# Kernel tuning notes

Hardware: AMD Instinct MI355X
Metric: run time of the kernel (lower is better)

## Reference

```python
import jax, jax.numpy as jnp
import numpy as np

N_TX, N_CARD, N_MERCH = 200000, 50000, 10000
E = 200000
TX_IN, EMB, H = 128, 64, 128
N_LAYERS, N_ETYPES = 2, 4  # etypes: 0 card->tx, 1 tx->card, 2 merch->tx, 3 tx->merch


def setup_inputs() -> dict:
    key = jax.random.key(0)
    ks = jax.random.split(key, 24)
    s = 0.05
    inp = {
        "tx_x": jax.random.normal(ks[0], (N_TX, TX_IN), jnp.float32),
        "card_ids": jnp.arange(N_CARD, dtype=jnp.int64),
        "merch_ids": jnp.arange(N_MERCH, dtype=jnp.int64),
        "e_card": jax.random.randint(ks[1], (E,), 0, N_CARD),
        "e_tx_c": jnp.arange(E, dtype=jnp.int64),
        "e_merch": jax.random.randint(ks[2], (E,), 0, N_MERCH),
        "e_tx_m": jnp.arange(E, dtype=jnp.int64),
        # parameters
        "card_emb": jax.random.normal(ks[3], (N_CARD, EMB), jnp.float32) * s,
        "merch_emb": jax.random.normal(ks[4], (N_MERCH, EMB), jnp.float32) * s,
        "card_proj_W": jax.random.normal(ks[5], (EMB, H), jnp.float32) * s,
        "card_proj_b": jnp.zeros((H,), jnp.float32),
        "merch_proj_W": jax.random.normal(ks[6], (EMB, H), jnp.float32) * s,
        "merch_proj_b": jnp.zeros((H,), jnp.float32),
        "tx_W": jax.random.normal(ks[7], (TX_IN, H), jnp.float32) * s,
        "tx_b": jnp.zeros((H,), jnp.float32),
        "conv_Wl": jax.random.normal(ks[8], (N_LAYERS, N_ETYPES, H, H), jnp.float32) * s,
        "conv_bl": jnp.zeros((N_LAYERS, N_ETYPES, H), jnp.float32),
        "conv_Wr": jax.random.normal(ks[9], (N_LAYERS, N_ETYPES, H, H), jnp.float32) * s,
        "h1_W": jax.random.normal(ks[10], (H, H), jnp.float32) * s,
        "h1_b": jnp.zeros((H,), jnp.float32),
        "h2_W": jax.random.normal(ks[11], (H, 1), jnp.float32) * s,
        "h2_b": jnp.zeros((1,), jnp.float32),
    }
    return inp


def _sage(x_src, x_dst, src, dst, Wl, bl, Wr, n_dst):
    # PyG SAGEConv: mean-aggregate neighbor features, then lin_l(agg)+lin_r(x_dst)
    agg = jax.ops.segment_sum(x_src[src], dst, num_segments=n_dst)
    cnt = jax.ops.segment_sum(jnp.ones((src.shape[0],), x_src.dtype), dst, num_segments=n_dst)
    mean = agg / jnp.maximum(cnt, 1.0)[:, None]
    return mean @ Wl + bl + x_dst @ Wr


def reference(tx_x, card_ids, merch_ids, e_card, e_tx_c, e_merch, e_tx_m,
              card_emb, merch_emb, card_proj_W, card_proj_b, merch_proj_W, merch_proj_b,
              tx_W, tx_b, conv_Wl, conv_bl, conv_Wr, h1_W, h1_b, h2_W, h2_b):
    # input encoders (dropout inactive at eval)
    h_tx = jax.nn.relu(tx_x @ tx_W + tx_b)
    h_card = card_emb[card_ids] @ card_proj_W + card_proj_b
    h_merch = merch_emb[merch_ids] @ merch_proj_W + merch_proj_b

    for l in range(N_LAYERS):
        Wl, bl, Wr = conv_Wl[l], conv_bl[l], conv_Wr[l]
        # HeteroConv aggr='sum' across edge types sharing a dst type
        o_tx = (_sage(h_card, h_tx, e_card, e_tx_c, Wl[0], bl[0], Wr[0], N_TX)
                + _sage(h_merch, h_tx, e_merch, e_tx_m, Wl[2], bl[2], Wr[2], N_TX))
        o_card = _sage(h_tx, h_card, e_tx_c, e_card, Wl[1], bl[1], Wr[1], N_CARD)
        o_merch = _sage(h_tx, h_merch, e_tx_m, e_merch, Wl[3], bl[3], Wr[3], N_MERCH)
        h_tx, h_card, h_merch = jax.nn.relu(o_tx), jax.nn.relu(o_card), jax.nn.relu(o_merch)

    logits = (jax.nn.relu(h_tx @ h1_W + h1_b) @ h2_W + h2_b).reshape(-1)
    return logits
```

## Files before the change

### kernel.cpp

```cpp
#include <hip/hip_runtime.h>


#define N_TX    200000
#define N_CARD  50000
#define N_MERCH 10000
#define NE      200000

typedef __attribute__((ext_vector_type(8))) short short8;
typedef __attribute__((ext_vector_type(4))) float f32x4;

__device__ inline unsigned short f2b(float f) {
    unsigned u = __builtin_bit_cast(unsigned, f);
    unsigned r = (u + 0x7fffu + ((u >> 16) & 1u)) >> 16;
    return (unsigned short)r;
}
__device__ inline float b2f(unsigned short s) {
    return __builtin_bit_cast(float, (unsigned)s << 16);
}

__global__ __launch_bounds__(256, 2) void mfma_gemm(
    const void* __restrict__ A1, int a1_f32, const int* __restrict__ rowIdx1,
    int K1, const unsigned short* __restrict__ WT1,
    const void* __restrict__ A2, int K2, const unsigned short* __restrict__ WT2,
    const float* __restrict__ bias,
    const unsigned short* __restrict__ P1, const int* __restrict__ I1,
    const unsigned short* __restrict__ P2, const int* __restrict__ I2,
    int do_relu, const float* __restrict__ h2W, const float* __restrict__ h2b,
    void* __restrict__ OUT, int M)
{
    __shared__ unsigned short WTs[128 * 136];
    const int tid  = threadIdx.x;
    const int wave = tid >> 6;
    const int lane = tid & 63;
    const int quad = lane >> 4;
    const int l15  = lane & 15;
    const int base = blockIdx.x * 128;

    f32x4 acc[2][8];
#pragma unroll
    for (int mt = 0; mt < 2; ++mt)
#pragma unroll
        for (int nt = 0; nt < 8; ++nt)
            acc[mt][nt] = (f32x4){0.f, 0.f, 0.f, 0.f};

    for (int pass = 0; pass < 2; ++pass) {
        const void* A = (pass == 0) ? A1 : A2;
        if (!A) break;
        const int K = (pass == 0) ? K1 : K2;
        const unsigned short* WTg = (pass == 0) ? WT1 : WT2;
        const int* rIdx = (pass == 0) ? rowIdx1 : nullptr;
        const int a_f32 = (pass == 0) ? a1_f32 : 0;
        const int stride = K + 8;
        const int nkk = K >> 5;
        const int ksh = (K == 128) ? 7 : 6;

        __syncthreads();
        for (int i = tid * 8; i < (K << 7); i += 2048) {
            int row = i >> ksh;
            int off = i & (K - 1);
            *reinterpret_cast<short8*>(&WTs[row * stride + off]) =
                *reinterpret_cast<const short8*>(WTg + i);
        }
        __syncthreads();

        short8 af[2][4];
#pragma unroll
        for (int mt = 0; mt < 2; ++mt) {
            int r = base + wave * 32 + mt * 16 + l15;
            int rc = (r < M) ? r : 0;
            int ar = rIdx ? rIdx[rc] : rc;
            if (a_f32) {
                const float* ap = (const float*)A + (size_t)ar * K + quad * 8;
#pragma unroll
                for (int kk = 0; kk < 4; ++kk) if (kk < nkk) {
                    float4 u = *reinterpret_cast<const float4*>(ap + kk * 32);
                    float4 v = *reinterpret_cast<const float4*>(ap + kk * 32 + 4);
                    short8 t;
                    t[0] = (short)f2b(u.x); t[1] = (short)f2b(u.y);
                    t[2] = (short)f2b(u.z); t[3] = (short)f2b(u.w);
                    t[4] = (short)f2b(v.x); t[5] = (short)f2b(v.y);
                    t[6] = (short)f2b(v.z); t[7] = (short)f2b(v.w);
                    af[mt][kk] = t;
                }
            } else {
                const unsigned short* ap =
                    (const unsigned short*)A + (size_t)ar * K + quad * 8;
#pragma unroll
                for (int kk = 0; kk < 4; ++kk) if (kk < nkk)
                    af[mt][kk] = *reinterpret_cast<const short8*>(ap + kk * 32);
            }
        }

#pragma unroll
        for (int nt = 0; nt < 8; ++nt) {
            short8 bf[4];
            const unsigned short* bp = &WTs[(nt * 16 + l15) * stride + quad * 8];
#pragma unroll
            for (int kk = 0; kk < 4; ++kk) if (kk < nkk)
                bf[kk] = *reinterpret_cast<const short8*>(bp + kk * 32);
#pragma unroll
            for (int mt = 0; mt < 2; ++mt)
#pragma unroll
                for (int kk = 0; kk < 4; ++kk) if (kk < nkk)
                    acc[mt][nt] = __builtin_amdgcn_mfma_f32_16x16x32_bf16(
                        af[mt][kk], bf[kk], acc[mt][nt], 0, 0, 0);
        }
    }

    __syncthreads();
#pragma unroll
    for (int mt = 0; mt < 2; ++mt) {
        int lrow0 = wave * 32 + mt * 16 + quad * 4;
#pragma unroll
        for (int nt = 0; nt < 8; ++nt) {
            int col = nt * 16 + l15;
#pragma unroll
            for (int reg = 0; reg < 4; ++reg)
                WTs[(lrow0 + reg) * 136 + col] = f2b(acc[mt][nt][reg]);
        }
    }
    __syncthreads();

    const int c0 = l15 * 8;
    float bias8[8], h2w8[8];
#pragma unroll
    for (int j = 0; j < 8; ++j) {
        bias8[j] = bias ? bias[c0 + j] : 0.f;
        h2w8[j]  = h2W  ? h2W[c0 + j]  : 0.f;
    }
    unsigned short* OUTb = (unsigned short*)OUT;
    float* OUTf = (float*)OUT;
    const int rgrp = tid >> 4;
#pragma unroll 4
    for (int p = 0; p < 8; ++p) {
        const int rloc = p * 16 + rgrp;
        const int r = base + rloc;
        const bool valid = r < M;
        const int rc = valid ? r : 0;
        short8 av = *reinterpret_cast<const short8*>(&WTs[rloc * 136 + c0]);
        short8 p1v{}, p2v{};
        if (P1) {
            size_t i1 = (size_t)I1[rc] * 128;
            p1v = *reinterpret_cast<const short8*>(P1 + i1 + c0);
        }
        if (P2) {
            size_t i2 = (size_t)I2[rc] * 128;
            p2v = *reinterpret_cast<const short8*>(P2 + i2 + c0);
        }
        float hsum = 0.f;
        short8 ov;
#pragma unroll
        for (int j = 0; j < 8; ++j) {
            float o = b2f((unsigned short)av[j]) + bias8[j];
            if (P1) o += b2f((unsigned short)p1v[j]);
            if (P2) o += b2f((unsigned short)p2v[j]);
            if (do_relu) o = fmaxf(o, 0.f);
            if (h2W) hsum += o * h2w8[j];
            else ov[j] = (short)f2b(o);
        }
        if (h2W) {
            hsum += __shfl_xor(hsum, 1);
            hsum += __shfl_xor(hsum, 2);
            hsum += __shfl_xor(hsum, 4);
            hsum += __shfl_xor(hsum, 8);
            if (l15 == 0 && valid) OUTf[r] = hsum + h2b[0];
        } else if (valid) {
            *reinterpret_cast<short8*>(OUTb + (size_t)r * 128 + c0) = ov;
        }
    }
}

__global__ __launch_bounds__(256) void convert_weights(
    const float* __restrict__ tx_W, const float* __restrict__ card_proj_W,
    const float* __restrict__ merch_proj_W, const float* __restrict__ h1_W,
    const float* __restrict__ conv_Wl, const float* __restrict__ conv_Wr,
    const float* __restrict__ conv_bl,
    unsigned short* __restrict__ WT, float* __restrict__ bsum)
{
    int job = blockIdx.y;
    int K = 128;
    const float* src = nullptr;
    const float* src2 = nullptr;
    if (job == 0) src = tx_W;
    else if (job == 1) { src = card_proj_W; K = 64; }
    else if (job == 2) { src = merch_proj_W; K = 64; }
    else if (job == 3) src = h1_W;
    else {
        int l = (job - 4) / 7, e = (job - 4) % 7;
        const float* Wl = conv_Wl + (size_t)l * 4 * 16384;
        const float* Wr = conv_Wr + (size_t)l * 4 * 16384;
        switch (e) {
            case 0: src = Wl; break;
            case 1: src = Wl + 16384; break;
            case 2: src = Wl + 2 * 16384; break;
            case 3: src = Wl + 3 * 16384; break;
            case 4: src = Wr + 16384; break;
            case 5: src = Wr + 3 * 16384; break;
            default:
                src = Wr; src2 = Wr + 2 * 16384;
                if (blockIdx.x == 0 && threadIdx.x < 128) {
                    const float* bl = conv_bl + (size_t)l * 4 * 128;
                    bsum[l * 128 + threadIdx.x] =
                        bl[threadIdx.x] + bl[2 * 128 + threadIdx.x];
                }
                break;
        }
    }
    int e = blockIdx.x * 256 + threadIdx.x;
    if (e < (K << 7)) {
        int n = (K == 128) ? (e >> 7) : (e >> 6);
        int k = e & (K - 1);
        float v = src[(size_t)k * 128 + n];
        if (src2) v += src2[(size_t)k * 128 + n];
        WT[(size_t)job * 16384 + n * K + k] = f2b(v);
    }
}

__global__ __launch_bounds__(256) void hist_kernel(
    const int* __restrict__ e_card, const int* __restrict__ e_merch,
    int* __restrict__ hist_c, int* __restrict__ hist_m, int E)
{
    int i = blockIdx.x * 256 + threadIdx.x;
    if (i < E) {
        atomicAdd(&hist_c[e_card[i]], 1);
        atomicAdd(&hist_m[e_merch[i]], 1);
    }
}

__global__ __launch_bounds__(1024) void scan2_kernel(
    const int* __restrict__ hist_c, int* __restrict__ offs_c, int* __restrict__ cur_c, int nc,
    const int* __restrict__ hist_m, int* __restrict__ offs_m, int* __restrict__ cur_m, int nm)
{
    const int* hist = (blockIdx.x == 0) ? hist_c : hist_m;
    int* offs = (blockIdx.x == 0) ? offs_c : offs_m;
    int* cursor = (blockIdx.x == 0) ? cur_c : cur_m;
    int n = (blockIdx.x == 0) ? nc : nm;
    __shared__ int wsum[16];
    __shared__ int s_carry;
    const int tid = threadIdx.x, lane = tid & 63, wid = tid >> 6;
    if (tid == 0) s_carry = 0;
    __syncthreads();
    for (int base = 0; base < n; base += 1024) {
        int i = base + tid;
        int v = (i < n) ? hist[i] : 0;
        int x = v;
#pragma unroll
        for (int d = 1; d < 64; d <<= 1) {
            int t = __shfl_up(x, d);
            if (lane >= d) x += t;
        }
        if (lane == 63) wsum[wid] = x;
        __syncthreads();
        if (wid == 0) {
            int y = (lane < 16) ? wsum[lane] : 0;
#pragma unroll
            for (int d = 1; d < 16; d <<= 1) {
                int t = __shfl_up(y, d);
                if (lane >= d) y += t;
            }
            if (lane < 16) wsum[lane] = y;
        }
        __syncthreads();
        int wbase = (wid > 0) ? wsum[wid - 1] : 0;
        int excl = s_carry + wbase + x - v;
        if (i < n) { offs[i] = excl; cursor[i] = excl; }
        __syncthreads();
        if (tid == 0) s_carry += wsum[15];
        __syncthreads();
    }
    if (threadIdx.x == 0) offs[n] = s_carry;
}

__global__ __launch_bounds__(256) void place_kernel(
    const int* __restrict__ e_card, const int* __restrict__ e_tx_c,
    const int* __restrict__ e_merch, const int* __restrict__ e_tx_m,
    int* __restrict__ cur_c, int* __restrict__ eidx_c,
    int* __restrict__ cur_m, int* __restrict__ eidx_m, int E)
{
    int i = blockIdx.x * 256 + threadIdx.x;
    if (i < E) {
        int pc = atomicAdd(&cur_c[e_card[i]], 1);
        eidx_c[pc] = e_tx_c[i];
        int pm = atomicAdd(&cur_m[e_merch[i]], 1);
        eidx_m[pm] = e_tx_m[i];
    }
}

__global__ __launch_bounds__(256) void gather_mean(
    const unsigned short* __restrict__ h_src, const int* __restrict__ offs,
    const int* __restrict__ eidx, unsigned short* __restrict__ out_mean, int n_dst)
{
    const int lane = threadIdx.x & 63;
    const int l15 = lane & 15;
    const int quad = lane >> 4;
    const int d = blockIdx.x * 4 + (threadIdx.x >> 6);
    if (d >= n_dst) return;
    const int s = offs[d], e = offs[d + 1];
    float a[8] = {0.f, 0.f, 0.f, 0.f, 0.f, 0.f, 0.f, 0.f};
    for (int p = s + quad; p < e; p += 4) {
        int tx = eidx[p];
        short8 v = *reinterpret_cast<const short8*>(
            h_src + (size_t)tx * 128 + l15 * 8);
#pragma unroll
        for (int j = 0; j < 8; ++j) a[j] += b2f((unsigned short)v[j]);
    }
#pragma unroll
    for (int j = 0; j < 8; ++j) {
        a[j] += __shfl_xor(a[j], 16);
        a[j] += __shfl_xor(a[j], 32);
    }
    if (quad == 0) {
        const float inv = (e > s) ? 1.0f / (float)(e - s) : 0.f;
        short8 o;
#pragma unroll
        for (int j = 0; j < 8; ++j) o[j] = (short)f2b(a[j] * inv);
        *reinterpret_cast<short8*>(out_mean + (size_t)d * 128 + l15 * 8) = o;
    }
}

extern "C" void kernel_launch(void* const* d_in, const int* in_sizes, int n_in,
                              void* d_out, int out_size, void* d_ws, size_t ws_size,
                              hipStream_t stream)
{
    const float* tx_x        = (const float*)d_in[0];
    const int*   card_ids    = (const int*)d_in[1];
    const int*   merch_ids   = (const int*)d_in[2];
    const int*   e_card      = (const int*)d_in[3];
    const int*   e_tx_c      = (const int*)d_in[4];
    const int*   e_merch     = (const int*)d_in[5];
    const int*   e_tx_m      = (const int*)d_in[6];
    const float* card_emb    = (const float*)d_in[7];
    const float* merch_emb   = (const float*)d_in[8];
    const float* card_proj_W = (const float*)d_in[9];
    const float* card_proj_b = (const float*)d_in[10];
    const float* merch_proj_W= (const float*)d_in[11];
    const float* merch_proj_b= (const float*)d_in[12];
    const float* tx_W        = (const float*)d_in[13];
    const float* tx_b        = (const float*)d_in[14];
    const float* conv_Wl     = (const float*)d_in[15];
    const float* conv_bl     = (const float*)d_in[16];
    const float* conv_Wr     = (const float*)d_in[17];
    const float* h1_W        = (const float*)d_in[18];
    const float* h1_b        = (const float*)d_in[19];
    const float* h2_W        = (const float*)d_in[20];
    const float* h2_b        = (const float*)d_in[21];

    char* wsb = (char*)d_ws;
    auto alloc = [&](size_t bytes) {
        char* p = wsb; wsb += (bytes + 255) & ~(size_t)255; return p;
    };
    unsigned short* h_tx       = (unsigned short*)alloc((size_t)N_TX * 128 * 2);
    unsigned short* h_card     = (unsigned short*)alloc((size_t)N_CARD * 128 * 2);
    unsigned short* h_merch    = (unsigned short*)alloc((size_t)N_MERCH * 128 * 2);
    unsigned short* p_card     = (unsigned short*)alloc((size_t)N_CARD * 128 * 2);
    unsigned short* p_merch    = (unsigned short*)alloc((size_t)N_MERCH * 128 * 2);
    unsigned short* mean_card  = (unsigned short*)alloc((size_t)N_CARD * 128 * 2);
    unsigned short* mean_merch = (unsigned short*)alloc((size_t)N_MERCH * 128 * 2);
    unsigned short* WT         = (unsigned short*)alloc((size_t)18 * 16384 * 2);
    float* bsum = (float*)alloc(2 * 128 * 4);
    int* hist_c = (int*)alloc((size_t)(N_CARD + N_MERCH) * 4);
    int* hist_m = hist_c + N_CARD;
    int* offs_c = (int*)alloc((size_t)(N_CARD + 1) * 4);
    int* cur_c  = (int*)alloc((size_t)N_CARD * 4);
    int* eidx_c = (int*)alloc((size_t)NE * 4);
    int* offs_m = (int*)alloc((size_t)(N_MERCH + 1) * 4);
    int* cur_m  = (int*)alloc((size_t)N_MERCH * 4);
    int* eidx_m = (int*)alloc((size_t)NE * 4);

    auto WTj = [&](int job) { return WT + (size_t)job * 16384; };

    auto gemm = [&](const void* A1, int a1f32, const int* ri, int K1,
                    const unsigned short* W1, const void* A2, int K2,
                    const unsigned short* W2, const float* bias,
                    const unsigned short* P1, const int* I1,
                    const unsigned short* P2, const int* I2, int relu,
                    const float* h2w, const float* h2bb, void* out, int M) {
        mfma_gemm<<<dim3((M + 127) / 128), dim3(256), 0, stream>>>(
            A1, a1f32, ri, K1, W1, A2, K2, W2, bias, P1, I1, P2, I2, relu,
            h2w, h2bb, out, M);
    };

    convert_weights<<<dim3(64, 18), dim3(256), 0, stream>>>(
        tx_W, card_proj_W, merch_proj_W, h1_W, conv_Wl, conv_Wr, conv_bl,
        WT, bsum);
    hipMemsetAsync(hist_c, 0, (size_t)(N_CARD + N_MERCH) * 4, stream);
    hist_kernel<<<dim3((NE + 255) / 256), dim3(256), 0, stream>>>(
        e_card, e_merch, hist_c, hist_m, NE);
    scan2_kernel<<<dim3(2), dim3(1024), 0, stream>>>(
        hist_c, offs_c, cur_c, N_CARD, hist_m, offs_m, cur_m, N_MERCH);
    place_kernel<<<dim3((NE + 255) / 256), dim3(256), 0, stream>>>(
        e_card, e_tx_c, e_merch, e_tx_m, cur_c, eidx_c, cur_m, eidx_m, NE);

    gemm(tx_x, 1, nullptr, 128, WTj(0), nullptr, 0, nullptr, tx_b,
         nullptr, nullptr, nullptr, nullptr, 1, nullptr, nullptr, h_tx, N_TX);
    gemm(card_emb, 1, card_ids, 64, WTj(1), nullptr, 0, nullptr, card_proj_b,
         nullptr, nullptr, nullptr, nullptr, 0, nullptr, nullptr, h_card, N_CARD);
    gemm(merch_emb, 1, merch_ids, 64, WTj(2), nullptr, 0, nullptr, merch_proj_b,
         nullptr, nullptr, nullptr, nullptr, 0, nullptr, nullptr, h_merch, N_MERCH);

    for (int l = 0; l < 2; ++l) {
        const float* bl = conv_bl + (size_t)l * 4 * 128;
        int j = 4 + l * 7;

        gather_mean<<<dim3((N_CARD + 3) / 4), dim3(256), 0, stream>>>(
            h_tx, offs_c, eidx_c, mean_card, N_CARD);
        gather_mean<<<dim3((N_MERCH + 3) / 4), dim3(256), 0, stream>>>(
            h_tx, offs_m, eidx_m, mean_merch, N_MERCH);

        gemm(h_card, 0, nullptr, 128, WTj(j + 0), nullptr, 0, nullptr, nullptr,
             nullptr, nullptr, nullptr, nullptr, 0, nullptr, nullptr, p_card, N_CARD);
        gemm(h_merch, 0, nullptr, 128, WTj(j + 2), nullptr, 0, nullptr, nullptr,
             nullptr, nullptr, nullptr, nullptr, 0, nullptr, nullptr, p_merch, N_MERCH);

        gemm(mean_card, 0, nullptr, 128, WTj(j + 1), h_card, 128, WTj(j + 4),
             bl + 1 * 128, nullptr, nullptr, nullptr, nullptr, 1,
             nullptr, nullptr, h_card, N_CARD);
        gemm(mean_merch, 0, nullptr, 128, WTj(j + 3), h_merch, 128, WTj(j + 5),
             bl + 3 * 128, nullptr, nullptr, nullptr, nullptr, 1,
             nullptr, nullptr, h_merch, N_MERCH);

        gemm(h_tx, 0, nullptr, 128, WTj(j + 6), nullptr, 0, nullptr,
             bsum + l * 128, p_card, e_card, p_merch, e_merch, 1,
             nullptr, nullptr, h_tx, N_TX);
    }

    gemm(h_tx, 0, nullptr, 128, WTj(3), nullptr, 0, nullptr, h1_b,
         nullptr, nullptr, nullptr, nullptr, 1, h2_W, h2_b, d_out, N_TX);
}
```

Measured before the change: 724.6 us.

## Read GEMM weights from global memory and prefetch epilogue gather rows early

New measurement: 825.9 us. 14.0% more time.

```diff
diff --git a/kernel.cpp b/kernel.cpp
--- a/kernel.cpp
+++ b/kernel.cpp
@@ -28,13 +28,30 @@
     int do_relu, const float* __restrict__ h2W, const float* __restrict__ h2b,
     void* __restrict__ OUT, int M)
 {
-    __shared__ unsigned short WTs[128 * 136];
+    __shared__ unsigned short Ts[128 * 136];
     const int tid  = threadIdx.x;
     const int wave = tid >> 6;
     const int lane = tid & 63;
     const int quad = lane >> 4;
     const int l15  = lane & 15;
     const int base = blockIdx.x * 128;
+    const int rgrp = tid >> 4;
+    const int c0   = l15 * 8;
+
+    int idx1[8], idx2[8];
+#pragma unroll
+    for (int p = 0; p < 8; ++p) {
+        int r = base + p * 16 + rgrp;
+        int rc = (r < M) ? r : 0;
+        idx1[p] = I1 ? I1[rc] : 0;
+        idx2[p] = I2 ? I2[rc] : 0;
+    }
+    float bias8[8], h2w8[8];
+#pragma unroll
+    for (int j = 0; j < 8; ++j) {
+        bias8[j] = bias ? bias[c0 + j] : 0.f;
+        h2w8[j]  = h2W  ? h2W[c0 + j]  : 0.f;
+    }
 
     f32x4 acc[2][8];
 #pragma unroll
@@ -50,18 +67,7 @@
         const unsigned short* WTg = (pass == 0) ? WT1 : WT2;
         const int* rIdx = (pass == 0) ? rowIdx1 : nullptr;
         const int a_f32 = (pass == 0) ? a1_f32 : 0;
-        const int stride = K + 8;
         const int nkk = K >> 5;
-        const int ksh = (K == 128) ? 7 : 6;
-
-        __syncthreads();
-        for (int i = tid * 8; i < (K << 7); i += 2048) {
-            int row = i >> ksh;
-            int off = i & (K - 1);
-            *reinterpret_cast<short8*>(&WTs[row * stride + off]) =
-                *reinterpret_cast<const short8*>(WTg + i);
-        }
-        __syncthreads();
 
         short8 af[2][4];
 #pragma unroll
@@ -94,7 +100,7 @@
 #pragma unroll
         for (int nt = 0; nt < 8; ++nt) {
             short8 bf[4];
-            const unsigned short* bp = &WTs[(nt * 16 + l15) * stride + quad * 8];
+            const unsigned short* bp = WTg + (nt * 16 + l15) * K + quad * 8;
 #pragma unroll
             for (int kk = 0; kk < 4; ++kk) if (kk < nkk)
                 bf[kk] = *reinterpret_cast<const short8*>(bp + kk * 32);
@@ -107,7 +113,6 @@
         }
     }
 
-    __syncthreads();
 #pragma unroll
     for (int mt = 0; mt < 2; ++mt) {
         int lrow0 = wave * 32 + mt * 16 + quad * 4;
@@ -116,44 +121,41 @@
             int col = nt * 16 + l15;
 #pragma unroll
             for (int reg = 0; reg < 4; ++reg)
-                WTs[(lrow0 + reg) * 136 + col] = f2b(acc[mt][nt][reg]);
-        }
-    }
+                Ts[(lrow0 + reg) * 136 + col] = f2b(acc[mt][nt][reg]);
+        }
+    }
+
+    short8 p1v[8], p2v[8];
+    if (P1) {
+#pragma unroll
+        for (int p = 0; p < 8; ++p)
+            p1v[p] = *reinterpret_cast<const short8*>(
+                P1 + (size_t)idx1[p] * 128 + c0);
+    }
+    if (P2) {
+#pragma unroll
+        for (int p = 0; p < 8; ++p)
+            p2v[p] = *reinterpret_cast<const short8*>(
+                P2 + (size_t)idx2[p] * 128 + c0);
+    }
+
     __syncthreads();
 
-    const int c0 = l15 * 8;
-    float bias8[8], h2w8[8];
-#pragma unroll
-    for (int j = 0; j < 8; ++j) {
-        bias8[j] = bias ? bias[c0 + j] : 0.f;
-        h2w8[j]  = h2W  ? h2W[c0 + j]  : 0.f;
-    }
     unsigned short* OUTb = (unsigned short*)OUT;
     float* OUTf = (float*)OUT;
-    const int rgrp = tid >> 4;
-#pragma unroll 4
+#pragma unroll
     for (int p = 0; p < 8; ++p) {
         const int rloc = p * 16 + rgrp;
         const int r = base + rloc;
         const bool valid = r < M;
-        const int rc = valid ? r : 0;
-        short8 av = *reinterpret_cast<const short8*>(&WTs[rloc * 136 + c0]);
-        short8 p1v{}, p2v{};
-        if (P1) {
-            size_t i1 = (size_t)I1[rc] * 128;
-            p1v = *reinterpret_cast<const short8*>(P1 + i1 + c0);
-        }
-        if (P2) {
-            size_t i2 = (size_t)I2[rc] * 128;
-            p2v = *reinterpret_cast<const short8*>(P2 + i2 + c0);
-        }
+        short8 av = *reinterpret_cast<const short8*>(&Ts[rloc * 136 + c0]);
         float hsum = 0.f;
         short8 ov;
 #pragma unroll
         for (int j = 0; j < 8; ++j) {
             float o = b2f((unsigned short)av[j]) + bias8[j];
-            if (P1) o += b2f((unsigned short)p1v[j]);
-            if (P2) o += b2f((unsigned short)p2v[j]);
+            if (P1) o += b2f((unsigned short)p1v[p][j]);
+            if (P2) o += b2f((unsigned short)p2v[p][j]);
             if (do_relu) o = fmaxf(o, 0.f);
             if (h2W) hsum += o * h2w8[j];
             else ov[j] = (short)f2b(o);
```
